# Performance work log

Measured on AMD Instinct MI355X. Metric: run time of the kernel, lower is better.

## Reference

```python
import jax, jax.numpy as jnp
import numpy as np
from math import floor, log2

DEPTH = 4
DIM = 1024
HEADS = 16
DIM_HEAD = 64
FF_MULT = 4
NUM_TOKENS = 32000
SEQ = 2048
MASK_VALUE = -1e10
EPS = 1e-5
ATTN_INNER = DIM_HEAD * HEADS            # 1024
FF_INNER = DIM * FF_MULT                 # 4096
FUSED = (ATTN_INNER, DIM_HEAD, DIM_HEAD, FF_INNER, FF_INNER)  # q, k, v, ff, ff_gate


def get_alibi_slopes(heads):
    def pow2_slopes(n):
        start = 2 ** (-2 ** (-(log2(n) - 3)))
        return [start * start ** i for i in range(n)]
    if log2(heads).is_integer():
        return pow2_slopes(heads)
    c = 2 ** floor(log2(heads))
    return pow2_slopes(c) + pow2_slopes(2 * c)[0::2][: heads - c]


def make_attn_bias(seq_len, heads, mask_value):
    # ALiBi variant used by this module: bias depends only on key position j
    slopes = np.array(get_alibi_slopes(heads), dtype=np.float32)[:, None, None]  # [h,1,1]
    bias = slopes * np.arange(seq_len, dtype=np.float32)[None, None, :]          # [h,1,j]
    bias = np.broadcast_to(bias, (heads, seq_len, seq_len))
    causal = np.tril(np.ones((seq_len, seq_len), dtype=bool))
    return jnp.asarray(np.where(causal, bias, mask_value), dtype=jnp.float32)


def rmsnorm(x, gamma):
    ssq = jnp.sum(jnp.square(x), axis=-1, keepdims=True)
    return jax.lax.rsqrt(ssq + EPS) * x * gamma * (x.shape[-1] ** 0.5)


def block(x, attn_bias, wi, attn_wo, ff_wo, gamma):
    h = rmsnorm(x, gamma)
    splits = np.cumsum(FUSED[:-1])
    q, k, v, ff, ff_gate = jnp.split(h @ wi, splits, axis=-1)
    b, n, _ = q.shape
    # multi-query attention: k, v have a single shared head of size DIM_HEAD
    q = q.reshape(b, n, HEADS, DIM_HEAD).transpose(0, 2, 1, 3) * (DIM_HEAD ** -0.5)
    sim = jnp.einsum('bhid,bjd->bhij', q, k) + attn_bias
    attn = jax.nn.softmax(sim, axis=-1)
    out = jnp.einsum('bhij,bjd->bhid', attn, v)
    out = out.transpose(0, 2, 1, 3).reshape(b, n, ATTN_INNER)
    attn_out = out @ attn_wo
    ff_out = (ff * jax.nn.swish(ff_gate)) @ ff_wo
    return attn_out + ff_out


def setup_inputs() -> dict:
    key = jax.random.key(0)
    ks = jax.random.split(key, 6)
    return {
        'tokens': jax.random.randint(ks[0], (1, SEQ), 0, NUM_TOKENS),
        'embedding': jax.random.normal(ks[1], (NUM_TOKENS, DIM), jnp.float32) * 0.02,
        'wi': jax.random.normal(ks[2], (DEPTH, DIM, sum(FUSED)), jnp.float32),
        'attn_wo': jax.random.normal(ks[3], (DEPTH, ATTN_INNER, DIM), jnp.float32),
        'ff_wo': jax.random.normal(ks[4], (DEPTH, FF_INNER, DIM), jnp.float32),
        'gammas': jnp.ones((DEPTH, DIM), jnp.float32),
        'final_gamma': jnp.ones((DIM,), jnp.float32),
    }


def reference(tokens, embedding, wi, attn_wo, ff_wo, gammas, final_gamma):
    n = tokens.shape[-1]
    attn_bias = make_attn_bias(SEQ, HEADS, MASK_VALUE)[..., :n, :n]
    x = embedding[tokens]                     # [b, n, dim]
    for l in range(DEPTH):
        x = block(x, attn_bias, wi[l], attn_wo[l], ff_wo[l], gammas[l]) + x
    x = rmsnorm(x, final_gamma)
    return x @ embedding.T                    # tied-embedding logits [b, n, vocab]
```

## Files before the change

### kernel.cpp

```cpp
#include <hip/hip_runtime.h>
#include <stdint.h>


typedef __attribute__((ext_vector_type(8))) __bf16 bf16x8;
typedef __attribute__((ext_vector_type(4))) __bf16 bf16x4;
typedef __attribute__((ext_vector_type(8))) short s16x8;
typedef __attribute__((ext_vector_type(4))) float f32x4;

#define SEQ   2048
#define DIM   1024
#define NHEAD 16
#define DHEAD 64
#define FUSEN 9344
#define QKW   1088
#define FFIN  4096
#define VOCAB 32000
#define AFW   5120
#define LOG2E 1.44269504f

__device__ __forceinline__ f32x4 mfma16(bf16x8 a, bf16x8 b, f32x4 c) {
  return __builtin_amdgcn_mfma_f32_16x16x32_bf16(
      __builtin_bit_cast(s16x8, a), __builtin_bit_cast(s16x8, b), c, 0, 0, 0);
}

__device__ __forceinline__ void load_lds16(const __bf16* g, __bf16* l) {
  __builtin_amdgcn_global_load_lds(
      (const __attribute__((address_space(1))) uint32_t*)g,
      (__attribute__((address_space(3))) uint32_t*)l, 16, 0, 0);
}


__global__ void cast_k(const float* __restrict__ in, __bf16* __restrict__ out, int n8) {
  int i = blockIdx.x * 256 + threadIdx.x;
  if (i >= n8) return;
  const float4* p = (const float4*)in + (size_t)i * 2;
  float4 a = p[0], b = p[1];
  bf16x8 o;
  o[0] = (__bf16)a.x; o[1] = (__bf16)a.y; o[2] = (__bf16)a.z; o[3] = (__bf16)a.w;
  o[4] = (__bf16)b.x; o[5] = (__bf16)b.y; o[6] = (__bf16)b.z; o[7] = (__bf16)b.w;
  *(bf16x8*)(out + (size_t)i * 8) = o;
}

__global__ void gather_k(const int* __restrict__ tokens, const float* __restrict__ emb,
                         float* __restrict__ x) {
  int n = blockIdx.x;
  int tok = tokens[n];
  float4 v = ((const float4*)(emb + (size_t)tok * DIM))[threadIdx.x];
  ((float4*)(x + (size_t)n * DIM))[threadIdx.x] = v;
}

__global__ __launch_bounds__(256) void transpose_cast_k(
    const float* __restrict__ in, __bf16* __restrict__ out, int R, int C, int ldo) {
  __shared__ float tile[32][33];
  int tx = threadIdx.x & 31, ty = threadIdx.x >> 5;
  int c0 = blockIdx.x * 32, r0 = blockIdx.y * 32;
  for (int i = ty; i < 32; i += 8)
    tile[i][tx] = in[(size_t)(r0 + i) * C + c0 + tx];
  __syncthreads();
  for (int i = ty; i < 32; i += 8)
    out[(size_t)(c0 + i) * ldo + r0 + tx] = (__bf16)tile[tx][i];
}

template <int HASP>
__global__ __launch_bounds__(256) void rmsnorm_fuse_k(
    const float* __restrict__ x, const float* __restrict__ p,
    const float* __restrict__ gamma, float* __restrict__ xn,
    __bf16* __restrict__ h) {
  int n = blockIdx.x;
  float4 v = ((const float4*)(x + (size_t)n * DIM))[threadIdx.x];
  if (HASP) {
    float4 a = ((const float4*)(p + (size_t)n * DIM))[threadIdx.x];
    float4 b = ((const float4*)(p + (size_t)(SEQ + n) * DIM))[threadIdx.x];
    v.x += a.x + b.x; v.y += a.y + b.y; v.z += a.z + b.z; v.w += a.w + b.w;
    ((float4*)(xn + (size_t)n * DIM))[threadIdx.x] = v;
  }
  float ssq = v.x * v.x + v.y * v.y + v.z * v.z + v.w * v.w;
  for (int m = 32; m >= 1; m >>= 1) ssq += __shfl_xor(ssq, m, 64);
  __shared__ float red[4];
  if ((threadIdx.x & 63) == 0) red[threadIdx.x >> 6] = ssq;
  __syncthreads();
  float tot = red[0] + red[1] + red[2] + red[3];
  float rs = rsqrtf(tot + 1e-5f) * 32.0f;
  float4 g = ((const float4*)gamma)[threadIdx.x];
  bf16x4 o;
  o[0] = (__bf16)(v.x * rs * g.x);
  o[1] = (__bf16)(v.y * rs * g.y);
  o[2] = (__bf16)(v.z * rs * g.z);
  o[3] = (__bf16)(v.w * rs * g.w);
  *(bf16x4*)(h + (size_t)n * DIM + threadIdx.x * 4) = o;
}

__global__ __launch_bounds__(256) void vtrans_k(const __bf16* __restrict__ hw,
                                                __bf16* __restrict__ vT) {
  __shared__ __bf16 tile[32][33];
  int tx = threadIdx.x & 31, ty = threadIdx.x >> 5;
  int j0 = blockIdx.x * 32, d0 = blockIdx.y * 32;
  for (int i = ty; i < 32; i += 8)
    tile[i][tx] = hw[(size_t)(j0 + i) * FUSEN + 1088 + d0 + tx];
  __syncthreads();
  for (int i = ty; i < 32; i += 8)
    vT[(size_t)(d0 + i) * SEQ + j0 + tx] = tile[tx][i];
}

__global__ void act_k(const __bf16* __restrict__ hw, __bf16* __restrict__ aof) {
  int n = blockIdx.y;
  int m = (blockIdx.x * 256 + threadIdx.x) * 8;
  bf16x8 f = *(const bf16x8*)(hw + (size_t)n * FUSEN + 1152 + m);
  bf16x8 g = *(const bf16x8*)(hw + (size_t)n * FUSEN + 5248 + m);
  bf16x8 o;
#pragma unroll
  for (int i = 0; i < 8; i++) {
    float ff = (float)f[i], gg = (float)g[i];
    float s = gg / (1.f + expf(-gg));
    o[i] = (__bf16)(ff * s);
  }
  *(bf16x8*)(aof + (size_t)n * AFW + 1024 + m) = o;
}

template <int MODE>
__global__ __launch_bounds__(256) void gemm_bt_k(
    const __bf16* __restrict__ A, int lda,
    const __bf16* __restrict__ Bt, int ldb,
    float* __restrict__ outf, int ldc,
    __bf16* __restrict__ qh, __bf16* __restrict__ ql, __bf16* __restrict__ hw,
    int K) {
  __shared__ __bf16 lA[8192];
  __shared__ __bf16 lB[8192];
  const int t = threadIdx.x;
  const int lane = t & 63, wave = t >> 6;
  const int lo4 = lane & 15, hi2 = lane >> 4;
  const int nwg = gridDim.x * gridDim.y;
  const int orig = blockIdx.y * gridDim.x + blockIdx.x;
  const int xcd = orig & 7, off = orig >> 3;
  const int qq = nwg >> 3, rr = nwg & 7;
  const int nid = (xcd < rr ? xcd * (qq + 1) : rr * (qq + 1) + (xcd - rr) * qq) + off;
  const int bm = nid % gridDim.y, bn = nid / gridDim.y;
  const int k0 = blockIdx.z * K;
  const int wr = (wave >> 1) * 64, wc = (wave & 1) * 64;

  f32x4 acc[4][4];
#pragma unroll
  for (int m = 0; m < 4; m++)
#pragma unroll
    for (int n = 0; n < 4; n++) acc[m][n] = f32x4{0.f, 0.f, 0.f, 0.f};

  const int e0 = t * 8;
  const int e1 = 2048 + t * 8;
  const __bf16* gA0 = A + (size_t)(bm * 128 + (e0 >> 5)) * lda + (e0 & 31) + k0;
  const __bf16* gA1 = A + (size_t)(bm * 128 + (e1 >> 5)) * lda + (e1 & 31) + k0;
  const __bf16* gB0 = Bt + (size_t)(bn * 128 + (e0 >> 5)) * ldb + (e0 & 31) + k0;
  const __bf16* gB1 = Bt + (size_t)(bn * 128 + (e1 >> 5)) * ldb + (e1 & 31) + k0;
  __bf16* dA0 = &lA[wave * 512];
  __bf16* dA1 = &lA[2048 + wave * 512];
  __bf16* dB0 = &lB[wave * 512];
  __bf16* dB1 = &lB[2048 + wave * 512];

  for (int kt = 0; kt < K; kt += 64) {
    load_lds16(gA0 + kt, dA0);
    load_lds16(gA1 + kt, dA1);
    load_lds16(gB0 + kt, dB0);
    load_lds16(gB1 + kt, dB1);
    load_lds16(gA0 + kt + 32, dA0 + 4096);
    load_lds16(gA1 + kt + 32, dA1 + 4096);
    load_lds16(gB0 + kt + 32, dB0 + 4096);
    load_lds16(gB1 + kt + 32, dB1 + 4096);
    __syncthreads();
#pragma unroll
    for (int half = 0; half < 2; half++) {
      const __bf16* sA = &lA[half * 4096];
      const __bf16* sB = &lB[half * 4096];
      bf16x8 af[4], bf_[4];
#pragma unroll
      for (int m = 0; m < 4; m++)
        af[m] = *(const bf16x8*)&sA[(wr + m * 16 + lo4) * 32 + hi2 * 8];
#pragma unroll
      for (int n = 0; n < 4; n++)
        bf_[n] = *(const bf16x8*)&sB[(wc + n * 16 + lo4) * 32 + hi2 * 8];
#pragma unroll
      for (int m = 0; m < 4; m++)
#pragma unroll
        for (int n = 0; n < 4; n++)
          acc[m][n] = mfma16(af[m], bf_[n], acc[m][n]);
    }
    __syncthreads();
  }

  float* op = outf + (size_t)blockIdx.z * SEQ * DIM;
#pragma unroll
  for (int m = 0; m < 4; m++) {
    const int rowb = bm * 128 + wr + m * 16 + hi2 * 4;
#pragma unroll
    for (int n = 0; n < 4; n++) {
      const int col = bn * 128 + wc + n * 16 + lo4;
#pragma unroll
      for (int j = 0; j < 4; j++) {
        const int row = rowb + j;
        float v = acc[m][n][j];
        if (MODE == 0) {
          __builtin_nontemporal_store(v, &op[(size_t)row * ldc + col]);
        } else {
          if (col < QKW) {
            __bf16 hi = (__bf16)v;
            qh[(size_t)row * QKW + col] = hi;
            ql[(size_t)row * QKW + col] = (__bf16)(v - (float)hi);
          } else {
            hw[(size_t)row * FUSEN + col] = (__bf16)v;
          }
        }
      }
    }
  }
}

__global__ __launch_bounds__(512, 1) void gemm256_k(
    const __bf16* __restrict__ A, const __bf16* __restrict__ Bt,
    float* __restrict__ C, int ldc, int K) {
  __shared__ __bf16 lds[65536];
  const int t = threadIdx.x;
  const int lane = t & 63, w = t >> 6;
  const int lo4 = lane & 15, hi2 = lane >> 4;
  const int wr = w >> 2, wc = w & 3;
  const int nwg = gridDim.x * gridDim.y;
  const int orig = blockIdx.y * gridDim.x + blockIdx.x;
  const int xcd = orig & 7, off = orig >> 3;
  const int qq = nwg >> 3, rr = nwg & 7;
  const int nid = (xcd < rr ? xcd * (qq + 1) : rr * (qq + 1) + (xcd - rr) * qq) + off;
  const int bm = nid % gridDim.y, bn = nid / gridDim.y;

  const int srow = lane >> 2;
  const int scol = ((lane & 3) * 8) ^ ((lane >> 5) << 4);
  const __bf16* gA = A + (size_t)(bm * 256 + srow) * K + scol;
  const __bf16* gB = Bt + (size_t)(bn * 256 + srow) * K + scol;
  const int cpr = (hi2 * 8) ^ ((lo4 >= 8) ? 16 : 0);

  auto STAGE = [&](int kt, int ks, int isB) {
    const __bf16* g = (isB ? gB : gA) + kt * 64 + ks * 32;
    __bf16* l = &lds[isB * 32768 + (kt & 1) * 16384 + ks * 8192 + (2 * w) * 512];
    load_lds16(g + (size_t)(2 * w) * 16 * K, l);
    load_lds16(g + (size_t)(2 * w + 1) * 16 * K, l + 512);
  };

  f32x4 acc[8][4];
#pragma unroll
  for (int m = 0; m < 8; m++)
#pragma unroll
    for (int n = 0; n < 4; n++) acc[m][n] = f32x4{0.f, 0.f, 0.f, 0.f};

  STAGE(0, 0, 0); STAGE(0, 0, 1); STAGE(0, 1, 0); STAGE(0, 1, 1);

  const int NIT = K >> 7;
  bf16x8 bfr[4];
  for (int it = 0; it < NIT; ++it) {
#pragma unroll
    for (int p = 0; p < 8; ++p) {
      const int g = p >> 2;
      const int u = p & 3;
      const int ks = u >> 1, mh = u & 1;
      const int kt = 2 * it + g;
      const bool dostage = (it < NIT - 1) || (g == 0);
      if ((u & 1) == 0) {
        if (it == NIT - 1 && g == 1 && u == 2)
          asm volatile("s_waitcnt vmcnt(0)" ::: "memory");
        else
          asm volatile("s_waitcnt vmcnt(4)" ::: "memory");
        __builtin_amdgcn_s_barrier();
      }
      const int abase = g * 16384 + ks * 8192 + lo4 * 32 + cpr;
      if ((u & 1) == 0) {
#pragma unroll
        for (int n = 0; n < 4; n++)
          bfr[n] = *(const bf16x8*)&lds[32768 + abase + (wc * 4 + n) * 512];
      }
      bf16x8 af[4];
#pragma unroll
      for (int mm = 0; mm < 4; mm++)
        af[mm] = *(const bf16x8*)&lds[abase + (wr * 8 + mh * 4 + mm) * 512];
      if (dostage) STAGE(kt + 1, ks, u & 1);
      __builtin_amdgcn_s_setprio(1);
#pragma unroll
      for (int mm = 0; mm < 4; mm++)
#pragma unroll
        for (int n = 0; n < 4; n++)
          acc[mh * 4 + mm][n] = mfma16(af[mm], bfr[n], acc[mh * 4 + mm][n]);
      __builtin_amdgcn_s_setprio(0);
    }
  }

#pragma unroll
  for (int m = 0; m < 8; m++) {
    const int rowb = bm * 256 + wr * 128 + m * 16 + hi2 * 4;
#pragma unroll
    for (int n = 0; n < 4; n++) {
      const int col = bn * 256 + wc * 64 + n * 16 + lo4;
#pragma unroll
      for (int j = 0; j < 4; j++)
        __builtin_nontemporal_store(acc[m][n][j], &C[(size_t)(rowb + j) * ldc + col]);
    }
  }
}

__global__ __launch_bounds__(256, 4) void flash_k(
    const __bf16* __restrict__ qh, const __bf16* __restrict__ ql,
    const __bf16* __restrict__ vT, __bf16* __restrict__ aof) {
  const int t = threadIdx.x;
  const int lane = t & 63, wave = t >> 6;
  const int lo4 = lane & 15, hi2 = lane >> 4;
  const int b = blockIdx.x;
  const int h = b & 15;
  const int s = b >> 4;
  const int pr = wave >> 1, half = wave & 1;
  const int c = pr ? (127 - s) : s;
  const int qrow0 = c * 16;
  const int nt = (c >> 2) + 1;
  const int ntA = (nt + 1) >> 1;
  const int jt0 = half ? ntA : 0;
  const int jtE = half ? nt : ntA;
  const float slope2 = exp2f(-0.5f * (float)(h + 1)) * LOG2E;
  const float scale2 = 0.125f * LOG2E;

  __shared__ __bf16 lP[4][16][72];
  __shared__ float smO[2][2][16][65];
  __shared__ float sml[2][2][16][2];
  __bf16 (*lPw)[72] = lP[wave];

  bf16x8 qhf[2], qlf[2];
#pragma unroll
  for (int kk = 0; kk < 2; kk++) {
    size_t qoff = (size_t)(qrow0 + lo4) * QKW + h * 64 + kk * 32 + hi2 * 8;
    qhf[kk] = *(const bf16x8*)(qh + qoff);
    qlf[kk] = *(const bf16x8*)(ql + qoff);
  }

  float jb[4][4];
#pragma unroll
  for (int f = 0; f < 4; f++)
#pragma unroll
    for (int r = 0; r < 4; r++)
      jb[f][r] = slope2 * (float)(jt0 * 64 + f * 16 + hi2 * 4 + r);
  const float dj = slope2 * 64.0f;
  const int iq = qrow0 + lo4;

  f32x4 O[4];
#pragma unroll
  for (int f = 0; f < 4; f++) O[f] = f32x4{0.f, 0.f, 0.f, 0.f};
  float mr = -1e30f, lr = 0.f;

  for (int jt = jt0; jt < jtE; ++jt) {
    f32x4 sc[4];
#pragma unroll
    for (int f = 0; f < 4; f++) sc[f] = f32x4{0.f, 0.f, 0.f, 0.f};
    __builtin_amdgcn_s_setprio(1);
#pragma unroll
    for (int kk = 0; kk < 2; kk++) {
#pragma unroll
      for (int f = 0; f < 4; f++) {
        size_t koff = (size_t)(jt * 64 + f * 16 + lo4) * QKW + 1024 + kk * 32 + hi2 * 8;
        bf16x8 khf = *(const bf16x8*)(qh + koff);
        bf16x8 klf = *(const bf16x8*)(ql + koff);
        sc[f] = mfma16(khf, qlf[kk], sc[f]);
        sc[f] = mfma16(klf, qhf[kk], sc[f]);
        sc[f] = mfma16(khf, qhf[kk], sc[f]);
      }
    }
    __builtin_amdgcn_s_setprio(0);

    float pv[4][4];
    float tmax = -1e30f;
#pragma unroll
    for (int f = 0; f < 4; f++)
#pragma unroll
      for (int r = 0; r < 4; r++) {
        const int j = jt * 64 + f * 16 + hi2 * 4 + r;
        float v = fmaf(sc[f][r], scale2, jb[f][r]);
        if (j > iq) v = -1e30f;
        pv[f][r] = v;
        tmax = fmaxf(tmax, v);
      }
    tmax = fmaxf(tmax, __shfl_xor(tmax, 16, 64));
    tmax = fmaxf(tmax, __shfl_xor(tmax, 32, 64));
    float mn = fmaxf(mr, tmax);
    float corr = exp2f(mr - mn);
    mr = mn;
    float rs = 0.f;
#pragma unroll
    for (int f = 0; f < 4; f++)
#pragma unroll
      for (int r = 0; r < 4; r++) {
        float pe = exp2f(pv[f][r] - mn);
        __bf16 pb = (__bf16)pe;
        lPw[lo4][f * 16 + hi2 * 4 + r] = pb;
        rs += (float)pb;
      }
    rs += __shfl_xor(rs, 16, 64);
    rs += __shfl_xor(rs, 32, 64);
    lr = lr * corr + rs;
    float co[4];
#pragma unroll
    for (int r = 0; r < 4; r++)
      co[r] = __shfl(corr, (lane & 48) + hi2 * 4 + r, 64);
#pragma unroll
    for (int f = 0; f < 4; f++)
#pragma unroll
      for (int r = 0; r < 4; r++) O[f][r] *= co[r];

    __builtin_amdgcn_s_setprio(1);
#pragma unroll
    for (int kk = 0; kk < 2; kk++) {
      bf16x8 pa = *(const bf16x8*)&lPw[lo4][kk * 32 + hi2 * 8];
#pragma unroll
      for (int f = 0; f < 4; f++) {
        bf16x8 vb = *(const bf16x8*)(vT + (size_t)(f * 16 + lo4) * SEQ + jt * 64 + kk * 32 + hi2 * 8);
        O[f] = mfma16(pa, vb, O[f]);
      }
    }
    __builtin_amdgcn_s_setprio(0);

#pragma unroll
    for (int f = 0; f < 4; f++)
#pragma unroll
      for (int r = 0; r < 4; r++) jb[f][r] += dj;
  }

#pragma unroll
  for (int f = 0; f < 4; f++)
#pragma unroll
    for (int r = 0; r < 4; r++)
      smO[pr][half][hi2 * 4 + r][f * 16 + lo4] = O[f][r];
  if (hi2 == 0) {
    sml[pr][half][lo4][0] = mr;
    sml[pr][half][lo4][1] = lr;
  }
  __syncthreads();
  if (half == 0) {
#pragma unroll
    for (int r = 0; r < 4; r++) {
      const int row = hi2 * 4 + r;
      float mA = sml[pr][0][row][0], lA = sml[pr][0][row][1];
      float mB = sml[pr][1][row][0], lB = sml[pr][1][row][1];
      float mS = fmaxf(mA, mB);
      float cA = exp2f(mA - mS), cB = exp2f(mB - mS);
      float li = lA * cA + lB * cB;
#pragma unroll
      for (int f = 0; f < 4; f++) {
        float v = (smO[pr][0][row][f * 16 + lo4] * cA +
                   smO[pr][1][row][f * 16 + lo4] * cB) / li;
        aof[(size_t)(qrow0 + row) * AFW + h * 64 + f * 16 + lo4] = (__bf16)v;
      }
    }
  }
}


extern "C" void kernel_launch(void* const* d_in, const int* in_sizes, int n_in,
                              void* d_out, int out_size, void* d_ws, size_t ws_size,
                              hipStream_t stream) {
  const int* tokens  = (const int*)d_in[0];
  const float* emb   = (const float*)d_in[1];
  const float* wi    = (const float*)d_in[2];
  const float* awo   = (const float*)d_in[3];
  const float* fwo   = (const float*)d_in[4];
  const float* gam   = (const float*)d_in[5];
  const float* fgam  = (const float*)d_in[6];
  float* out = (float*)d_out;

  char* wsp = (char*)d_ws;
  size_t woff = 0;
  auto walloc = [&](size_t b) { void* p = wsp + woff; woff += (b + 255) & ~(size_t)255; return p; };
  __bf16* embb = (__bf16*)walloc((size_t)VOCAB * DIM * 2);
  __bf16* wiT  = (__bf16*)walloc((size_t)FUSEN * DIM * 2);
  __bf16* BT2  = (__bf16*)walloc((size_t)DIM * AFW * 2);
  __bf16* h    = (__bf16*)walloc((size_t)SEQ * DIM * 2);

  char* op = (char*)d_out;
  size_t ooff = 0;
  auto oalloc = [&](size_t b) { void* p = op + ooff; ooff += (b + 255) & ~(size_t)255; return p; };
  float*  xA    = (float*)oalloc((size_t)SEQ * DIM * 4);
  float*  xB    = (float*)oalloc((size_t)SEQ * DIM * 4);
  float*  pp    = (float*)oalloc((size_t)2 * SEQ * DIM * 4);
  __bf16* hw    = (__bf16*)oalloc((size_t)SEQ * FUSEN * 2);
  __bf16* qhb   = (__bf16*)oalloc((size_t)SEQ * QKW * 2);
  __bf16* qlb   = (__bf16*)oalloc((size_t)SEQ * QKW * 2);
  __bf16* vT    = (__bf16*)oalloc((size_t)DHEAD * SEQ * 2);
  __bf16* aof   = (__bf16*)oalloc((size_t)SEQ * AFW * 2);
  (void)ws_size; (void)in_sizes; (void)n_in; (void)out_size;

  cast_k<<<(VOCAB * DIM / 8 + 255) / 256, 256, 0, stream>>>(emb, embb, VOCAB * DIM / 8);
  gather_k<<<SEQ, 256, 0, stream>>>(tokens, emb, xA);

  float* x = xA;
  float* xn = xB;
  for (int l = 0; l < 4; l++) {
    transpose_cast_k<<<dim3(FUSEN / 32, DIM / 32), 256, 0, stream>>>(
        wi + (size_t)l * DIM * FUSEN, wiT, DIM, FUSEN, DIM);
    transpose_cast_k<<<dim3(DIM / 32, DIM / 32), 256, 0, stream>>>(
        awo + (size_t)l * DIM * DIM, BT2, DIM, DIM, AFW);
    transpose_cast_k<<<dim3(DIM / 32, FFIN / 32), 256, 0, stream>>>(
        fwo + (size_t)l * FFIN * DIM, BT2 + 1024, FFIN, DIM, AFW);

    if (l == 0) {
      rmsnorm_fuse_k<0><<<SEQ, 256, 0, stream>>>(x, nullptr, gam, nullptr, h);
    } else {
      rmsnorm_fuse_k<1><<<SEQ, 256, 0, stream>>>(x, pp, gam + l * DIM, xn, h);
      float* tmp = x; x = xn; xn = tmp;
    }
    gemm_bt_k<1><<<dim3(FUSEN / 128, SEQ / 128), 256, 0, stream>>>(
        h, DIM, wiT, DIM, nullptr, 0, qhb, qlb, hw, DIM);
    vtrans_k<<<dim3(SEQ / 32, DHEAD / 32), 256, 0, stream>>>(hw, vT);
    flash_k<<<dim3(1024), 256, 0, stream>>>(qhb, qlb, vT, aof);
    act_k<<<dim3(FFIN / 2048, SEQ), 256, 0, stream>>>(hw, aof);
    gemm_bt_k<0><<<dim3(DIM / 128, SEQ / 128, 2), 256, 0, stream>>>(
        aof, AFW, BT2, AFW, pp, DIM, nullptr, nullptr, nullptr, AFW / 2);
  }

  rmsnorm_fuse_k<1><<<SEQ, 256, 0, stream>>>(x, pp, fgam, xn, h);
  gemm256_k<<<dim3(VOCAB / 256, SEQ / 256), 512, 0, stream>>>(
      h, embb, out, VOCAB, DIM);
}
```

Baseline: 1.270 ms.

## Fuse V transpose and SwiGLU into QKV GEMM epilogue, batch weight transposes

```diff
diff --git a/kernel.cpp b/kernel.cpp
--- a/kernel.cpp
+++ b/kernel.cpp
@@ -49,16 +49,41 @@
   ((float4*)(x + (size_t)n * DIM))[threadIdx.x] = v;
 }
 
-__global__ __launch_bounds__(256) void transpose_cast_k(
-    const float* __restrict__ in, __bf16* __restrict__ out, int R, int C, int ldo) {
+__device__ __forceinline__ int permcol(int c) {
+  if (c < 1152) return c;
+  if (c < 5248) { int i = c - 1152; return 1152 + ((i >> 4) << 5) + (i & 15); }
+  int i = c - 5248; return 1152 + ((i >> 4) << 5) + 16 + (i & 15);
+}
+
+__global__ __launch_bounds__(256) void transpose_wi_k(
+    const float* __restrict__ in, __bf16* __restrict__ out) {
   __shared__ float tile[32][33];
+  int l = blockIdx.z;
   int tx = threadIdx.x & 31, ty = threadIdx.x >> 5;
   int c0 = blockIdx.x * 32, r0 = blockIdx.y * 32;
+  const float* inl = in + (size_t)l * DIM * FUSEN;
+  __bf16* outl = out + (size_t)l * FUSEN * DIM;
   for (int i = ty; i < 32; i += 8)
-    tile[i][tx] = in[(size_t)(r0 + i) * C + c0 + tx];
+    tile[i][tx] = inl[(size_t)(r0 + i) * FUSEN + c0 + tx];
   __syncthreads();
   for (int i = ty; i < 32; i += 8)
-    out[(size_t)(c0 + i) * ldo + r0 + tx] = (__bf16)tile[tx][i];
+    outl[(size_t)permcol(c0 + i) * DIM + r0 + tx] = (__bf16)tile[tx][i];
+}
+
+__global__ __launch_bounds__(256) void transpose_b_k(
+    const float* __restrict__ in, __bf16* __restrict__ out,
+    int R, int C, int ldo, int co, size_t outLstride) {
+  __shared__ float tile[32][33];
+  int l = blockIdx.z;
+  int tx = threadIdx.x & 31, ty = threadIdx.x >> 5;
+  int c0 = blockIdx.x * 32, r0 = blockIdx.y * 32;
+  const float* inl = in + (size_t)l * R * C;
+  __bf16* outl = out + (size_t)l * outLstride;
+  for (int i = ty; i < 32; i += 8)
+    tile[i][tx] = inl[(size_t)(r0 + i) * C + c0 + tx];
+  __syncthreads();
+  for (int i = ty; i < 32; i += 8)
+    outl[(size_t)(c0 + i) * ldo + co + r0 + tx] = (__bf16)tile[tx][i];
 }
 
 template <int HASP>
@@ -90,39 +115,13 @@
   *(bf16x4*)(h + (size_t)n * DIM + threadIdx.x * 4) = o;
 }
 
-__global__ __launch_bounds__(256) void vtrans_k(const __bf16* __restrict__ hw,
-                                                __bf16* __restrict__ vT) {
-  __shared__ __bf16 tile[32][33];
-  int tx = threadIdx.x & 31, ty = threadIdx.x >> 5;
-  int j0 = blockIdx.x * 32, d0 = blockIdx.y * 32;
-  for (int i = ty; i < 32; i += 8)
-    tile[i][tx] = hw[(size_t)(j0 + i) * FUSEN + 1088 + d0 + tx];
-  __syncthreads();
-  for (int i = ty; i < 32; i += 8)
-    vT[(size_t)(d0 + i) * SEQ + j0 + tx] = tile[tx][i];
-}
-
-__global__ void act_k(const __bf16* __restrict__ hw, __bf16* __restrict__ aof) {
-  int n = blockIdx.y;
-  int m = (blockIdx.x * 256 + threadIdx.x) * 8;
-  bf16x8 f = *(const bf16x8*)(hw + (size_t)n * FUSEN + 1152 + m);
-  bf16x8 g = *(const bf16x8*)(hw + (size_t)n * FUSEN + 5248 + m);
-  bf16x8 o;
-#pragma unroll
-  for (int i = 0; i < 8; i++) {
-    float ff = (float)f[i], gg = (float)g[i];
-    float s = gg / (1.f + expf(-gg));
-    o[i] = (__bf16)(ff * s);
-  }
-  *(bf16x8*)(aof + (size_t)n * AFW + 1024 + m) = o;
-}
-
 template <int MODE>
 __global__ __launch_bounds__(256) void gemm_bt_k(
     const __bf16* __restrict__ A, int lda,
     const __bf16* __restrict__ Bt, int ldb,
     float* __restrict__ outf, int ldc,
-    __bf16* __restrict__ qh, __bf16* __restrict__ ql, __bf16* __restrict__ hw,
+    __bf16* __restrict__ qh, __bf16* __restrict__ ql,
+    __bf16* __restrict__ vT, __bf16* __restrict__ aof,
     int K) {
   __shared__ __bf16 lA[8192];
   __shared__ __bf16 lB[8192];
@@ -185,27 +184,61 @@
     __syncthreads();
   }
 
-  float* op = outf + (size_t)blockIdx.z * SEQ * DIM;
-#pragma unroll
-  for (int m = 0; m < 4; m++) {
-    const int rowb = bm * 128 + wr + m * 16 + hi2 * 4;
-#pragma unroll
-    for (int n = 0; n < 4; n++) {
-      const int col = bn * 128 + wc + n * 16 + lo4;
-#pragma unroll
-      for (int j = 0; j < 4; j++) {
-        const int row = rowb + j;
-        float v = acc[m][n][j];
-        if (MODE == 0) {
-          __builtin_nontemporal_store(v, &op[(size_t)row * ldc + col]);
-        } else {
-          if (col < QKW) {
-            __bf16 hi = (__bf16)v;
-            qh[(size_t)row * QKW + col] = hi;
-            ql[(size_t)row * QKW + col] = (__bf16)(v - (float)hi);
-          } else {
-            hw[(size_t)row * FUSEN + col] = (__bf16)v;
-          }
+  if (MODE == 0) {
+    float* op = outf + (size_t)blockIdx.z * SEQ * DIM;
+#pragma unroll
+    for (int m = 0; m < 4; m++) {
+      const int rowb = bm * 128 + wr + m * 16 + hi2 * 4;
+#pragma unroll
+      for (int n = 0; n < 4; n++) {
+        const int col = bn * 128 + wc + n * 16 + lo4;
+#pragma unroll
+        for (int j = 0; j < 4; j++)
+          __builtin_nontemporal_store(acc[m][n][j], &op[(size_t)(rowb + j) * ldc + col]);
+      }
+    }
+  } else if (bn < 8 || (bn == 8 && wc == 0)) {
+#pragma unroll
+    for (int m = 0; m < 4; m++) {
+      const int rowb = bm * 128 + wr + m * 16 + hi2 * 4;
+#pragma unroll
+      for (int n = 0; n < 4; n++) {
+        const int col = bn * 128 + wc + n * 16 + lo4;
+#pragma unroll
+        for (int j = 0; j < 4; j++) {
+          float v = acc[m][n][j];
+          __bf16 hi = (__bf16)v;
+          qh[(size_t)(rowb + j) * QKW + col] = hi;
+          ql[(size_t)(rowb + j) * QKW + col] = (__bf16)(v - (float)hi);
+        }
+      }
+    }
+  } else if (bn == 8) {
+#pragma unroll
+    for (int m = 0; m < 4; m++) {
+      const int rowb = bm * 128 + wr + m * 16 + hi2 * 4;
+#pragma unroll
+      for (int n = 0; n < 4; n++) {
+        const int vcol = n * 16 + lo4;
+#pragma unroll
+        for (int j = 0; j < 4; j++)
+          vT[(size_t)vcol * SEQ + rowb + j] = (__bf16)acc[m][n][j];
+      }
+    }
+  } else {
+#pragma unroll
+    for (int m = 0; m < 4; m++) {
+      const int rowb = bm * 128 + wr + m * 16 + hi2 * 4;
+#pragma unroll
+      for (int np = 0; np < 4; np += 2) {
+        const int cb = (bn - 9) * 128 + wc + np * 16;
+        const int acol = 1024 + ((cb >> 5) << 4) + lo4;
+#pragma unroll
+        for (int j = 0; j < 4; j++) {
+          float ff = acc[m][np][j];
+          float gg = acc[m][np + 1][j];
+          float s = gg / (1.f + expf(-gg));
+          aof[(size_t)(rowb + j) * AFW + acol] = (__bf16)(ff * s);
         }
       }
     }
@@ -467,8 +500,6 @@
   size_t woff = 0;
   auto walloc = [&](size_t b) { void* p = wsp + woff; woff += (b + 255) & ~(size_t)255; return p; };
   __bf16* embb = (__bf16*)walloc((size_t)VOCAB * DIM * 2);
-  __bf16* wiT  = (__bf16*)walloc((size_t)FUSEN * DIM * 2);
-  __bf16* BT2  = (__bf16*)walloc((size_t)DIM * AFW * 2);
   __bf16* h    = (__bf16*)walloc((size_t)SEQ * DIM * 2);
 
   char* op = (char*)d_out;
@@ -477,26 +508,25 @@
   float*  xA    = (float*)oalloc((size_t)SEQ * DIM * 4);
   float*  xB    = (float*)oalloc((size_t)SEQ * DIM * 4);
   float*  pp    = (float*)oalloc((size_t)2 * SEQ * DIM * 4);
-  __bf16* hw    = (__bf16*)oalloc((size_t)SEQ * FUSEN * 2);
   __bf16* qhb   = (__bf16*)oalloc((size_t)SEQ * QKW * 2);
   __bf16* qlb   = (__bf16*)oalloc((size_t)SEQ * QKW * 2);
   __bf16* vT    = (__bf16*)oalloc((size_t)DHEAD * SEQ * 2);
   __bf16* aof   = (__bf16*)oalloc((size_t)SEQ * AFW * 2);
+  __bf16* wiT4  = (__bf16*)oalloc((size_t)4 * FUSEN * DIM * 2);
+  __bf16* BT24  = (__bf16*)oalloc((size_t)4 * DIM * AFW * 2);
   (void)ws_size; (void)in_sizes; (void)n_in; (void)out_size;
 
   cast_k<<<(VOCAB * DIM / 8 + 255) / 256, 256, 0, stream>>>(emb, embb, VOCAB * DIM / 8);
   gather_k<<<SEQ, 256, 0, stream>>>(tokens, emb, xA);
+  transpose_wi_k<<<dim3(FUSEN / 32, DIM / 32, 4), 256, 0, stream>>>(wi, wiT4);
+  transpose_b_k<<<dim3(DIM / 32, DIM / 32, 4), 256, 0, stream>>>(
+      awo, BT24, DIM, DIM, AFW, 0, (size_t)DIM * AFW);
+  transpose_b_k<<<dim3(DIM / 32, FFIN / 32, 4), 256, 0, stream>>>(
+      fwo, BT24, FFIN, DIM, AFW, 1024, (size_t)DIM * AFW);
 
   float* x = xA;
   float* xn = xB;
   for (int l = 0; l < 4; l++) {
-    transpose_cast_k<<<dim3(FUSEN / 32, DIM / 32), 256, 0, stream>>>(
-        wi + (size_t)l * DIM * FUSEN, wiT, DIM, FUSEN, DIM);
-    transpose_cast_k<<<dim3(DIM / 32, DIM / 32), 256, 0, stream>>>(
-        awo + (size_t)l * DIM * DIM, BT2, DIM, DIM, AFW);
-    transpose_cast_k<<<dim3(DIM / 32, FFIN / 32), 256, 0, stream>>>(
-        fwo + (size_t)l * FFIN * DIM, BT2 + 1024, FFIN, DIM, AFW);
-
     if (l == 0) {
       rmsnorm_fuse_k<0><<<SEQ, 256, 0, stream>>>(x, nullptr, gam, nullptr, h);
     } else {
@@ -504,12 +534,12 @@
       float* tmp = x; x = xn; xn = tmp;
     }
     gemm_bt_k<1><<<dim3(FUSEN / 128, SEQ / 128), 256, 0, stream>>>(
-        h, DIM, wiT, DIM, nullptr, 0, qhb, qlb, hw, DIM);
-    vtrans_k<<<dim3(SEQ / 32, DHEAD / 32), 256, 0, stream>>>(hw, vT);
+        h, DIM, wiT4 + (size_t)l * FUSEN * DIM, DIM, nullptr, 0,
+        qhb, qlb, vT, aof, DIM);
     flash_k<<<dim3(1024), 256, 0, stream>>>(qhb, qlb, vT, aof);
-    act_k<<<dim3(FFIN / 2048, SEQ), 256, 0, stream>>>(hw, aof);
     gemm_bt_k<0><<<dim3(DIM / 128, SEQ / 128, 2), 256, 0, stream>>>(
-        aof, AFW, BT2, AFW, pp, DIM, nullptr, nullptr, nullptr, AFW / 2);
+        aof, AFW, BT24 + (size_t)l * DIM * AFW, AFW, pp, DIM,
+        nullptr, nullptr, nullptr, nullptr, AFW / 2);
   }
 
   rmsnorm_fuse_k<1><<<SEQ, 256, 0, stream>>>(x, pp, fgam, xn, h);
```

New measurement: 1.219 ms. 1.04x faster.
